# Kernel tuning notes

Measured on AMD Instinct MI355X. Metric: run time of the kernel, lower is better.

The kernel has to match this reference:

```python
import jax, jax.numpy as jnp
import numpy as np

EPS = 1e-5  # torch BatchNorm1d default eps
N0, N, ORIG, F, K, H, NC = 16, 96, 92, 64, 41, 128, 3


def _bn(x, g, b, axes):
    # training-mode batchnorm: biased batch stats over `axes`, per-channel affine
    m = jnp.mean(x, axis=axes, keepdims=True)
    v = jnp.mean((x - m) ** 2, axis=axes, keepdims=True)
    return (x - m) / jnp.sqrt(v + EPS) * g + b


def setup_inputs() -> dict:
    key = jax.random.key(0)
    ks = jax.random.split(key, 16)
    s = 0.05
    return {
        "atom_fea": jax.random.normal(ks[0], (N0, N, ORIG), jnp.float32),
        "nbr_fea": jax.random.normal(ks[1], (N0, N, N, K), jnp.float32),
        "adj": jax.random.randint(ks[2], (N0, N, N), 0, 2, jnp.int64),
        "emb_W": jax.random.normal(ks[3], (ORIG, F), jnp.float32) * s,
        "emb_b": jnp.zeros((F,), jnp.float32),
        "conv_W": jax.random.normal(ks[4], (NC, 2 * F + K, 2 * F), jnp.float32) * s,
        "conv_b": jnp.zeros((NC, 2 * F), jnp.float32),
        "bn1_g": jnp.ones((NC, 2 * F), jnp.float32),
        "bn1_b": jnp.zeros((NC, 2 * F), jnp.float32),
        "bn2_g": jnp.ones((NC, F), jnp.float32),
        "bn2_b": jnp.zeros((NC, F), jnp.float32),
        "fc_W": jax.random.normal(ks[5], (F, H), jnp.float32) * s,
        "fc_b": jnp.zeros((H,), jnp.float32),
        "out_W": jax.random.normal(ks[6], (H, 1), jnp.float32) * s,
        "out_b": jnp.zeros((1,), jnp.float32),
    }


def reference(atom_fea, nbr_fea, adj, emb_W, emb_b, conv_W, conv_b,
              bn1_g, bn1_b, bn2_g, bn2_b, fc_W, fc_b, out_W, out_b):
    fea = atom_fea @ emb_W + emb_b                       # (N0, N, F)
    adjf = adj.astype(fea.dtype)[..., None]              # (N0, N, N, 1)
    for i in range(NC):
        # NOTE: faithful to source - both FEA and masked term broadcast atom j's
        # own features along the neighbor axis (unsqueeze(2) in torch code).
        FEA = jnp.broadcast_to(fea[:, :, None, :], (N0, N, N, F))
        total = jnp.concatenate([FEA, adjf * FEA, nbr_fea], axis=3)   # (N0,N,N,2F+K)
        gated = total @ conv_W[i] + conv_b[i]                         # (N0,N,N,2F)
        gated = _bn(gated, bn1_g[i], bn1_b[i], (0, 1, 2))
        filt, core = jnp.split(gated, 2, axis=3)
        summed = jnp.sum(jax.nn.sigmoid(filt) * jax.nn.softplus(core), axis=2)  # (N0,N,F)
        summed = _bn(summed, bn2_g[i], bn2_b[i], (0, 1))
        fea = jax.nn.softplus(fea + summed)
    crys = jnp.mean(fea, axis=1)                                      # (N0, F)
    crys = jax.nn.softplus(jax.nn.softplus(crys) @ fc_W + fc_b)       # (N0, H)
    return crys @ out_W + out_b                                       # (N0, 1)
```

## Files before the change

kernel.cpp:

```cpp
#include <hip/hip_runtime.h>
#include <math.h>

#define N0c   16
#define NAt   96
#define ORIG  92
#define Fc    64
#define Kc    41
#define Hc    128
#define NCc   3
#define C2    128
#define EPSBN 1e-5f
#define JG    4
#define JPW   (NAt / JG)
#define NREP  32
#define SRL_STRIDE 12288
#define AROW  72
#define WFRAG 16384
#define INV1  (1.f / (float)(N0c * NAt * NAt))
#define INV2  (1.f / (float)(N0c * NAt))

typedef __attribute__((ext_vector_type(8))) short short8_t;
typedef __attribute__((ext_vector_type(4))) float f32x4;

__device__ __forceinline__ float sp_(float x){
    return fmaxf(x, 0.f) + __logf(1.f + __expf(-fabsf(x)));
}
__device__ __forceinline__ float sgm_(float x){
    return 1.f / (1.f + __expf(-x));
}
__device__ __forceinline__ unsigned short bfhi(float x){
    union { float f; unsigned u; } v; v.f = x;
    unsigned r = v.u + 0x7fff + ((v.u >> 16) & 1);
    return (unsigned short)(r >> 16);
}
__device__ __forceinline__ float bf2f(unsigned short h){
    union { float f; unsigned u; } v; v.u = ((unsigned)h) << 16; return v.f;
}

__global__ __launch_bounds__(256) void k_embed(const float* __restrict__ atom,
                                               const float* __restrict__ W,
                                               const float* __restrict__ b,
                                               float* __restrict__ fea){
    int row = blockIdx.x * 4 + (threadIdx.x >> 6);
    int f   = threadIdx.x & 63;
    const float* ar = atom + row * ORIG;
    float acc = b[f];
    #pragma unroll 4
    for (int o = 0; o < ORIG; ++o) acc += ar[o] * W[o * Fc + f];
    fea[row * Fc + f] = acc;
}

__global__ __launch_bounds__(256) void k_pre(const float* __restrict__ nbr,
                                             const int*   __restrict__ adj,
                                             float* __restrict__ ST,
                                             float* __restrict__ cntf){
    int r    = blockIdx.x;
    int lane = threadIdx.x & 63;
    int jg   = __builtin_amdgcn_readfirstlane(threadIdx.x >> 6);
    __shared__ float rS[JG][Kc], rT[JG][Kc], rc[JG];
    float S = 0.f, T = 0.f, cn = 0.f;
    int j0 = jg * JPW;
    for (int j = j0; j < j0 + JPW; ++j){
        float a = (float)adj[r * NAt + j];
        float v = (lane < Kc) ? nbr[((size_t)r * NAt + j) * Kc + lane] : 0.f;
        S += v; T += a * v; cn += a;
    }
    if (lane < Kc){ rS[jg][lane] = S; rT[jg][lane] = T; }
    if (lane == 0) rc[jg] = cn;
    __syncthreads();
    int t = threadIdx.x;
    if (t < Kc){
        ST[r * (2 * Kc) + t]      = rS[0][t] + rS[1][t] + rS[2][t] + rS[3][t];
        ST[r * (2 * Kc) + Kc + t] = rT[0][t] + rT[1][t] + rT[2][t] + rT[3][t];
    }
    if (t == 0) cntf[r] = rc[0] + rc[1] + rc[2] + rc[3];
}

__global__ __launch_bounds__(128) void k_gram(const float* __restrict__ nbr,
                                              float* __restrict__ pG, int rpb){
    int blk = blockIdx.x;
    int t   = threadIdx.x;
    int k   = (t % 21) * 2;
    int lb  = (t / 21) * 7;
    __shared__ float L[NAt * Kc];
    float a0[7] = {0,0,0,0,0,0,0}, a1[7] = {0,0,0,0,0,0,0};
    for (int rr = 0; rr < rpb; ++rr){
        int r = blk * rpb + rr;
        __syncthreads();
        for (int i = t; i < NAt * Kc; i += 128)
            L[i] = nbr[(size_t)r * NAt * Kc + i];
        __syncthreads();
        if (t < 126){
            for (int j = 0; j < NAt; ++j){
                float vk0 = L[j * Kc + k];
                float vk1 = (k + 1 < Kc) ? L[j * Kc + k + 1] : 0.f;
                #pragma unroll
                for (int m = 0; m < 7; ++m){
                    if (lb + m < Kc){
                        float lv = L[j * Kc + lb + m];
                        a0[m] += vk0 * lv;
                        a1[m] += vk1 * lv;
                    }
                }
            }
        }
    }
    if (t < 126){
        float* dst = pG + (size_t)blk * (Kc * Kc);
        #pragma unroll
        for (int m = 0; m < 7; ++m){
            if (lb + m < Kc){
                dst[k * Kc + lb + m] = a0[m];
                if (k + 1 < Kc) dst[(k + 1) * Kc + lb + m] = a1[m];
            }
        }
    }
}

__global__ __launch_bounds__(64) void k_gred(const float* __restrict__ pG,
                                             float* __restrict__ G){
    int i  = (blockIdx.x % 27) * 64 + threadIdx.x;
    int b0 = (blockIdx.x / 27) * 96;
    if (i < Kc * Kc){
        float s = 0.f;
        #pragma unroll 4
        for (int b = b0; b < b0 + 96; ++b) s += pG[(size_t)b * (Kc * Kc) + i];
        atomicAdd(&G[i], s);
    }
}

__global__ void k_wt(const float* __restrict__ convW, float* __restrict__ W3T){
    int l = blockIdx.x, c = threadIdx.x;
    const float* Wl = convW + (size_t)l * 169 * C2;
    float* dst = W3T + ((size_t)l * C2 + c) * 44;
    for (int k = 0; k < Kc; ++k) dst[k] = Wl[(C2 + k) * C2 + c];
    dst[41] = 0.f; dst[42] = 0.f; dst[43] = 0.f;
}

__global__ __launch_bounds__(256) void k_wtb(const float* __restrict__ convW,
                                             unsigned short* __restrict__ W3F){
    int l = blockIdx.x;
    const float* Wl = convW + (size_t)l * 169 * C2;
    for (int it = 0; it < 8; ++it){
        int idx  = threadIdx.x + it * 256;
        int lane = idx & 63;
        int fid  = idx >> 6;
        int h    = fid & 1;
        int ks   = (fid >> 1) & 1;
        int nt   = fid >> 2;
        int n    = nt * 16 + (lane & 15);
        unsigned short* dst = W3F + (size_t)l * WFRAG + fid * 512 + lane * 8;
        #pragma unroll
        for (int i = 0; i < 8; ++i){
            int k = ks * 32 + (lane >> 4) * 8 + i;
            float w = (k < Kc) ? Wl[(C2 + k) * C2 + n] : 0.f;
            unsigned short hi = bfhi(w);
            dst[i] = h ? bfhi(w - bf2f(hi)) : hi;
        }
    }
}

__global__ __launch_bounds__(128) void k_quad(const float* __restrict__ G,
                                              const float* __restrict__ convW,
                                              float* __restrict__ q3){
    int l = blockIdx.x, c = threadIdx.x;
    const float* Wl = convW + (size_t)l * 169 * C2;
    __shared__ float GL[Kc * Kc];
    for (int i = c; i < Kc * Kc; i += 128) GL[i] = G[i];
    float w3[Kc];
    #pragma unroll
    for (int k = 0; k < Kc; ++k) w3[k] = Wl[(C2 + k) * C2 + c];
    __syncthreads();
    float q = 0.f;
    for (int k = 0; k < Kc; ++k){
        float gw = 0.f;
        #pragma unroll
        for (int m = 0; m < Kc; ++m) gw += GL[k * Kc + m] * w3[m];
        q += w3[k] * gw;
    }
    q3[l * C2 + c] = q;
}

__global__ __launch_bounds__(128)
void k_front(float* __restrict__ fea,
             const float* __restrict__ Wl,
             const float* __restrict__ bl,
             const float* __restrict__ W3Tl,
             const float* __restrict__ ST,
             const float* __restrict__ cntf,
             float* __restrict__ p1,
             float* __restrict__ p2,
             float* __restrict__ sum1R,
             float* __restrict__ sq1R,
             const float* __restrict__ summed,
             const float* __restrict__ sum2Rp,
             const float* __restrict__ sq2Rp,
             const float* __restrict__ g2p,
             const float* __restrict__ b2p,
             int upd){
    int c  = threadIdx.x;
    int r0 = blockIdx.x * 2;
    __shared__ float F2[2][Fc];
    __shared__ float A2L[Fc], B2L[Fc];

    if (upd){
        if (c < Fc){
            float s = 0.f, q = 0.f;
            for (int rr = 0; rr < NREP; ++rr){
                s += sum2Rp[rr * Fc + c];
                q += sq2Rp[rr * Fc + c];
            }
            float m = s * INV2;
            float v = q * INV2 - m * m;
            float A = g2p[c] * rsqrtf(v + EPSBN);
            A2L[c] = A;
            B2L[c] = b2p[c] - m * A;
        }
        __syncthreads();
        {
            int rr = c >> 6, cc = c & 63;
            int r  = r0 + rr;
            float nv = sp_(fea[r * Fc + cc] + summed[r * Fc + cc] * A2L[cc] + B2L[cc]);
            F2[rr][cc] = nv;
            fea[r * Fc + cc] = nv;
        }
        __syncthreads();
    } else {
        int rr = c >> 6, cc = c & 63;
        F2[rr][cc] = fea[(r0 + rr) * Fc + cc];
        __syncthreads();
    }

    float w3[Kc];
    const float* wt = W3Tl + c * 44;
    #pragma unroll
    for (int k = 0; k < 40; k += 4){
        float4 v = *(const float4*)(wt + k);
        w3[k] = v.x; w3[k+1] = v.y; w3[k+2] = v.z; w3[k+3] = v.w;
    }
    w3[40] = wt[40];
    float s1 = 0.f, q1 = 0.f;
    for (int rr = 0; rr < 2; ++rr){
        int r = r0 + rr;
        float a1 = bl[c], a2 = 0.f;
        #pragma unroll 8
        for (int f = 0; f < Fc; ++f){
            float fv = F2[rr][f];
            a1 += fv * Wl[f * C2 + c];
            a2 += fv * Wl[(Fc + f) * C2 + c];
        }
        p1[r * C2 + c] = a1;
        p2[r * C2 + c] = a2;
        const float* Sr = ST + r * (2 * Kc);
        const float* Tr = Sr + Kc;
        float u = 0.f, tt = 0.f;
        #pragma unroll
        for (int k = 0; k < Kc; ++k){ u += Sr[k] * w3[k]; tt += Tr[k] * w3[k]; }
        float cn = cntf[r];
        s1 += (float)NAt * a1 + cn * a2 + u;
        q1 += (float)NAt * a1 * a1 + cn * a2 * a2
            + 2.f * cn * a1 * a2 + 2.f * a1 * u + 2.f * a2 * tt;
    }
    int slot = blockIdx.x & (NREP - 1);
    atomicAdd(&sum1R[slot * C2 + c], s1);
    atomicAdd(&sq1R[slot * C2 + c], q1);
}

__global__ __launch_bounds__(512)
void k_apply(const float* __restrict__ nbr,
             const int*   __restrict__ adj,
             const unsigned short* __restrict__ W3Fl,
             const float* __restrict__ p1,
             const float* __restrict__ p2,
             const float* __restrict__ sum1R,
             const float* __restrict__ sq1R,
             const float* __restrict__ qv,
             const float* __restrict__ g1,
             const float* __restrict__ b1,
             float* __restrict__ summed,
             float* __restrict__ sum2R,
             float* __restrict__ sq2R){
    int r    = blockIdx.x;
    int tid  = threadIdx.x;
    int lane = tid & 63;
    int w    = __builtin_amdgcn_readfirstlane(tid >> 6);
    int ntF  = w & 3;
    int mh   = w >> 2;

    __shared__ unsigned short sAH[NAt * AROW];
    __shared__ unsigned short sAL[NAt * AROW];
    __shared__ float AJ[NAt];
    __shared__ float PL1[C2], PL2[C2], A1L[C2], B1L[C2];
    __shared__ float TpW[8][16];

    short8_t BH[2][2], BL[2][2];
    #pragma unroll
    for (int ni = 0; ni < 2; ++ni){
        int nt = ntF + ni * 4;
        #pragma unroll
        for (int ks = 0; ks < 2; ++ks){
            int fidH = (nt * 2 + ks) * 2;
            BH[ni][ks] = *(const short8_t*)(W3Fl + fidH * 512 + lane * 8);
            BL[ni][ks] = *(const short8_t*)(W3Fl + (fidH + 1) * 512 + lane * 8);
        }
    }

    const float* nb = nbr + (size_t)r * (NAt * Kc);
    for (int idx = tid; idx < NAt * Kc; idx += 512){
        int j = idx / Kc, k = idx - j * Kc;
        float x = nb[idx];
        unsigned short hi = bfhi(x);
        sAH[j * AROW + k] = hi;
        sAL[j * AROW + k] = bfhi(x - bf2f(hi));
    }
    for (int idx = tid; idx < NAt * 23; idx += 512){
        int j = idx / 23, k = Kc + (idx - j * 23);
        sAH[j * AROW + k] = 0;
        sAL[j * AROW + k] = 0;
    }
    if (tid < C2){
        int c = tid;
        float s = 0.f, q = 0.f;
        for (int rr = 0; rr < NREP; ++rr){ s += sum1R[rr * C2 + c]; q += sq1R[rr * C2 + c]; }
        float m = s * INV1;
        float v = (q + qv[c]) * INV1 - m * m;
        float A = g1[c] * rsqrtf(v + EPSBN);
        A1L[c] = A;
        B1L[c] = b1[c] - m * A;
    } else if (tid < 256){
        PL1[tid - 128] = p1[r * C2 + tid - 128];
    } else if (tid < 384){
        PL2[tid - 256] = p2[r * C2 + tid - 256];
    } else if (tid < 480){
        AJ[tid - 384] = (float)adj[r * NAt + tid - 384];
    }
    __syncthreads();

    f32x4 acc[3][2] = {};
    int q4 = (lane >> 4) * 8;
    #pragma unroll
    for (int mt = 0; mt < 3; ++mt){
        int jrow = (mh * 48 + mt * 16 + (lane & 15)) * AROW;
        short8_t AH0 = *(const short8_t*)(&sAH[jrow + q4]);
        short8_t AH1 = *(const short8_t*)(&sAH[jrow + 32 + q4]);
        short8_t AL0 = *(const short8_t*)(&sAL[jrow + q4]);
        short8_t AL1 = *(const short8_t*)(&sAL[jrow + 32 + q4]);
        #pragma unroll
        for (int ni = 0; ni < 2; ++ni){
            acc[mt][ni] = __builtin_amdgcn_mfma_f32_16x16x32_bf16(AH0, BH[ni][0], acc[mt][ni], 0, 0, 0);
            acc[mt][ni] = __builtin_amdgcn_mfma_f32_16x16x32_bf16(AH0, BL[ni][0], acc[mt][ni], 0, 0, 0);
            acc[mt][ni] = __builtin_amdgcn_mfma_f32_16x16x32_bf16(AL0, BH[ni][0], acc[mt][ni], 0, 0, 0);
            acc[mt][ni] = __builtin_amdgcn_mfma_f32_16x16x32_bf16(AH1, BH[ni][1], acc[mt][ni], 0, 0, 0);
            acc[mt][ni] = __builtin_amdgcn_mfma_f32_16x16x32_bf16(AH1, BL[ni][1], acc[mt][ni], 0, 0, 0);
            acc[mt][ni] = __builtin_amdgcn_mfma_f32_16x16x32_bf16(AL1, BH[ni][1], acc[mt][ni], 0, 0, 0);
        }
    }

    int cF = ntF * 16 + (lane & 15);
    int cC = cF + 64;
    float p1F = PL1[cF], p2F = PL2[cF], A1F = A1L[cF], B1F = B1L[cF];
    float p1C = PL1[cC], p2C = PL2[cC], A1C = A1L[cC], B1C = B1L[cC];
    float tsum = 0.f;
    #pragma unroll
    for (int mt = 0; mt < 3; ++mt){
        #pragma unroll
        for (int rg = 0; rg < 4; ++rg){
            int j = mh * 48 + mt * 16 + (lane >> 4) * 4 + rg;
            float ajf = AJ[j];
            float gf = (p1F + ajf * p2F + acc[mt][0][rg]) * A1F + B1F;
            float gc = (p1C + ajf * p2C + acc[mt][1][rg]) * A1C + B1C;
            tsum += sgm_(gf) * sp_(gc);
        }
    }
    tsum += __shfl_xor(tsum, 16);
    tsum += __shfl_xor(tsum, 32);
    if (lane < 16) TpW[w][lane] = tsum;
    __syncthreads();
    if (tid < Fc){
        int f = tid;
        float s = TpW[f >> 4][f & 15] + TpW[(f >> 4) + 4][f & 15];
        summed[r * Fc + f] = s;
        int slot = blockIdx.x & (NREP - 1);
        atomicAdd(&sum2R[slot * Fc + f], s);
        atomicAdd(&sq2R[slot * Fc + f], s * s);
    }
}

__global__ __launch_bounds__(128) void k_final(const float* __restrict__ fea,
                                               const float* __restrict__ summed,
                                               const float* __restrict__ sum2R,
                                               const float* __restrict__ sq2R,
                                               const float* __restrict__ g2,
                                               const float* __restrict__ b2,
                                               const float* __restrict__ fcW,
                                               const float* __restrict__ fcb,
                                               const float* __restrict__ outW,
                                               const float* __restrict__ outb,
                                               float* __restrict__ out){
    int b = blockIdx.x;
    int t = threadIdx.x;
    __shared__ float spc[Fc];
    __shared__ float red[Hc];
    if (t < Fc){
        float s = 0.f, q = 0.f;
        for (int r = 0; r < NREP; ++r){ s += sum2R[r * Fc + t]; q += sq2R[r * Fc + t]; }
        float m  = s * INV2;
        float v  = q * INV2 - m * m;
        float A2 = g2[t] * rsqrtf(v + EPSBN);
        float B2 = b2[t] - m * A2;
        float acc = 0.f;
        for (int i = 0; i < NAt; ++i){
            int idx = (b * NAt + i) * Fc + t;
            acc += sp_(fea[idx] + summed[idx] * A2 + B2);
        }
        spc[t] = sp_(acc * (1.f / NAt));
    }
    __syncthreads();
    float h = fcb[t];
    #pragma unroll 4
    for (int f = 0; f < Fc; ++f) h += spc[f] * fcW[f * Hc + t];
    h = sp_(h);
    red[t] = h * outW[t];
    __syncthreads();
    for (int off = 64; off > 0; off >>= 1){
        if (t < off) red[t] += red[t + off];
        __syncthreads();
    }
    if (t == 0) out[b] = red[0] + outb[0];
}

extern "C" void kernel_launch(void* const* d_in, const int* in_sizes, int n_in,
                              void* d_out, int out_size, void* d_ws, size_t ws_size,
                              hipStream_t stream){
    const float* atom  = (const float*)d_in[0];
    const float* nbr   = (const float*)d_in[1];
    const int*   adj   = (const int*)  d_in[2];
    const float* embW  = (const float*)d_in[3];
    const float* embB  = (const float*)d_in[4];
    const float* convW = (const float*)d_in[5];
    const float* convB = (const float*)d_in[6];
    const float* bn1g  = (const float*)d_in[7];
    const float* bn1b  = (const float*)d_in[8];
    const float* bn2g  = (const float*)d_in[9];
    const float* bn2b  = (const float*)d_in[10];
    const float* fcW   = (const float*)d_in[11];
    const float* fcb   = (const float*)d_in[12];
    const float* outW  = (const float*)d_in[13];
    const float* outb  = (const float*)d_in[14];
    float* out = (float*)d_out;
    float* ws  = (float*)d_ws;

    const int ROWS = N0c * NAt;
    float* fea    = ws;
    float* p1     = ws + 98304;
    float* p2     = ws + 294912;
    float* summed = ws + 491520;
    float* SRL    = ws + 589824;
    float* ST     = ws + 626688;
    float* cntf   = ws + 752640;
    float* q3     = ws + 754176;
    float* W3T    = ws + 754560;
    unsigned short* W3F = (unsigned short*)(ws + 771456);
    const size_t PERS = 796032;

    size_t ws_f = ws_size / sizeof(float);
    int nblk; float *pG, *G;
    if (ws_f >= PERS + (size_t)1536 * 1681 + 1681 + 64){
        nblk = 1536; pG = ws + PERS; G = pG + (size_t)nblk * 1681;
    } else if (ws_f >= PERS + (size_t)768 * 1681 + 1681 + 64){
        nblk = 768;  pG = ws + PERS; G = pG + (size_t)nblk * 1681;
    } else if (ws_f >= PERS + (size_t)384 * 1681 + 1681 + 64){
        nblk = 384;  pG = ws + PERS; G = pG + (size_t)nblk * 1681;
    } else {
        nblk = 384;  pG = ws;        G = ws + 650000;
    }
    int rpb = 1536 / nblk;
    int ph  = nblk / 96;

    hipMemsetAsync(G, 0, Kc * Kc * sizeof(float), stream);
    k_gram <<<nblk, 128, 0, stream>>>(nbr, pG, rpb);
    k_gred <<<27 * ph, 64, 0, stream>>>(pG, G);
    k_wt   <<<NCc, C2, 0, stream>>>(convW, W3T);
    k_wtb  <<<NCc, 256, 0, stream>>>(convW, W3F);
    k_quad <<<NCc, C2, 0, stream>>>(G, convW, q3);
    k_embed<<<ROWS / 4, 256, 0, stream>>>(atom, embW, embB, fea);
    k_pre  <<<ROWS, 256, 0, stream>>>(nbr, adj, ST, cntf);
    hipMemsetAsync(SRL, 0, 3 * SRL_STRIDE * sizeof(float), stream);

    for (int l = 0; l < NCc; ++l){
        const float* Wl   = convW + (size_t)l * 169 * C2;
        const float* bl   = convB + l * C2;
        const float* W3Tl = W3T + (size_t)l * C2 * 44;
        const unsigned short* W3Fl = W3F + (size_t)l * WFRAG;
        float* sum1R = SRL + l * SRL_STRIDE;
        float* sq1R  = sum1R + 4096;
        float* sum2R = sum1R + 8192;
        float* sq2R  = sum1R + 10240;
        const float* sum2Rp = (l > 0) ? SRL + (l - 1) * SRL_STRIDE + 8192 : SRL;
        const float* sq2Rp  = (l > 0) ? SRL + (l - 1) * SRL_STRIDE + 10240 : SRL;
        const float* g2p    = bn2g + (l > 0 ? (l - 1) : 0) * Fc;
        const float* b2p    = bn2b + (l > 0 ? (l - 1) : 0) * Fc;

        k_front <<<ROWS / 2, C2, 0, stream>>>(fea, Wl, bl, W3Tl, ST, cntf,
                                              p1, p2, sum1R, sq1R,
                                              summed, sum2Rp, sq2Rp, g2p, b2p,
                                              l > 0 ? 1 : 0);
        k_apply <<<ROWS, 512, 0, stream>>>(nbr, adj, W3Fl, p1, p2,
                                           sum1R, sq1R, q3 + l * C2,
                                           bn1g + l * C2, bn1b + l * C2,
                                           summed, sum2R, sq2R);
    }

    k_final<<<N0c, Hc, 0, stream>>>(fea, summed,
                                    SRL + 2 * SRL_STRIDE + 8192,
                                    SRL + 2 * SRL_STRIDE + 10240,
                                    bn2g + 2 * Fc, bn2b + 2 * Fc,
                                    fcW, fcb, outW, outb, out);
}
```

Baseline: 292.6 us.

## Replace scalar per-row front kernel with split-bf16 MFMA block GEMM

Replaces the scalar k_front kernel, which runs two rows per 128-thread block, with k_pgemm. The new kernel processes 16 rows per 512-thread block and computes p1, p2 and the nbr projections u and tt as one GEMM on bf16 MFMA instructions. Three-term hi/lo bf16 splitting keeps the result close to fp32 accuracy. A new prep kernel packs the weights into MFMA fragment layout, and BN1 partial stats are reduced with shuffles before the atomics. This is meant to cut the front-stage compute cost, at the price of extra prep work and some precision loss from the bf16 split.

```diff
diff --git a/kernel.cpp b/kernel.cpp
--- a/kernel.cpp
+++ b/kernel.cpp
@@ -16,6 +16,9 @@
 #define SRL_STRIDE 12288
 #define AROW  72
 #define WFRAG 16384
+#define PROW  200
+#define DROW  516
+#define PGFRAG (32 * 2 * 2 * 512)
 #define INV1  (1.f / (float)(N0c * NAt * NAt))
 #define INV2  (1.f / (float)(N0c * NAt))
 
@@ -129,14 +132,6 @@
     }
 }
 
-__global__ void k_wt(const float* __restrict__ convW, float* __restrict__ W3T){
-    int l = blockIdx.x, c = threadIdx.x;
-    const float* Wl = convW + (size_t)l * 169 * C2;
-    float* dst = W3T + ((size_t)l * C2 + c) * 44;
-    for (int k = 0; k < Kc; ++k) dst[k] = Wl[(C2 + k) * C2 + c];
-    dst[41] = 0.f; dst[42] = 0.f; dst[43] = 0.f;
-}
-
 __global__ __launch_bounds__(256) void k_wtb(const float* __restrict__ convW,
                                              unsigned short* __restrict__ W3F){
     int l = blockIdx.x;
@@ -160,6 +155,32 @@
     }
 }
 
+__global__ __launch_bounds__(64) void k_wtb2(const float* __restrict__ convW,
+                                             unsigned short* __restrict__ W3F2){
+    int l  = blockIdx.x >> 5;
+    int nt = blockIdx.x & 31;
+    const float* Wl = convW + (size_t)l * 169 * C2;
+    int lane = threadIdx.x;
+    int kb = (nt < 16) ? 0 : (nt < 24 ? 64 : 128);
+    for (int f = 0; f < 4; ++f){
+        int ks2 = f >> 1, h = f & 1;
+        unsigned short* dst = W3F2 + (size_t)l * PGFRAG
+                            + (((size_t)nt * 2 + ks2) * 2 + h) * 512 + lane * 8;
+        #pragma unroll
+        for (int i = 0; i < 8; ++i){
+            int kabs = kb + ks2 * 32 + (lane >> 4) * 8 + i;
+            int n    = nt * 16 + (lane & 15);
+            float wv = 0.f;
+            if (nt < 8)        wv = Wl[kabs * C2 + n];
+            else if (nt < 16)  wv = Wl[(64 + kabs) * C2 + (n - 128)];
+            else if (nt < 24){ int kk = kabs - 64;  if (kk < Kc) wv = Wl[(C2 + kk) * C2 + (n - 256)]; }
+            else             { int kk = kabs - 128; if (kk < Kc) wv = Wl[(C2 + kk) * C2 + (n - 384)]; }
+            unsigned short hi = bfhi(wv);
+            dst[i] = h ? bfhi(wv - bf2f(hi)) : hi;
+        }
+    }
+}
+
 __global__ __launch_bounds__(128) void k_quad(const float* __restrict__ G,
                                               const float* __restrict__ convW,
                                               float* __restrict__ q3){
@@ -181,89 +202,129 @@
     q3[l * C2 + c] = q;
 }
 
-__global__ __launch_bounds__(128)
-void k_front(float* __restrict__ fea,
-             const float* __restrict__ Wl,
+__global__ __launch_bounds__(512)
+void k_pgemm(float* __restrict__ fea,
              const float* __restrict__ bl,
-             const float* __restrict__ W3Tl,
+             const unsigned short* __restrict__ Bf,
              const float* __restrict__ ST,
              const float* __restrict__ cntf,
-             float* __restrict__ p1,
-             float* __restrict__ p2,
-             float* __restrict__ sum1R,
-             float* __restrict__ sq1R,
              const float* __restrict__ summed,
              const float* __restrict__ sum2Rp,
              const float* __restrict__ sq2Rp,
              const float* __restrict__ g2p,
              const float* __restrict__ b2p,
+             float* __restrict__ p1,
+             float* __restrict__ p2,
+             float* __restrict__ sum1R,
+             float* __restrict__ sq1R,
              int upd){
-    int c  = threadIdx.x;
-    int r0 = blockIdx.x * 2;
-    __shared__ float F2[2][Fc];
-    __shared__ float A2L[Fc], B2L[Fc];
-
-    if (upd){
-        if (c < Fc){
-            float s = 0.f, q = 0.f;
-            for (int rr = 0; rr < NREP; ++rr){
-                s += sum2Rp[rr * Fc + c];
-                q += sq2Rp[rr * Fc + c];
+    int r0   = blockIdx.x * 16;
+    int tid  = threadIdx.x;
+    int lane = tid & 63;
+    int w    = __builtin_amdgcn_readfirstlane(tid >> 6);
+    __shared__ unsigned short AH[16 * PROW], AL[16 * PROW];
+    __shared__ float Db[16 * DROW];
+    __shared__ float A2L[Fc], B2L[Fc], cnL[16];
+
+    if (upd && tid < Fc){
+        float s = 0.f, q = 0.f;
+        for (int rr = 0; rr < NREP; ++rr){
+            s += sum2Rp[rr * Fc + tid];
+            q += sq2Rp[rr * Fc + tid];
+        }
+        float m = s * INV2;
+        float v = q * INV2 - m * m;
+        float A = g2p[tid] * rsqrtf(v + EPSBN);
+        A2L[tid] = A;
+        B2L[tid] = b2p[tid] - m * A;
+    }
+    if (tid < 16) cnL[tid] = cntf[r0 + tid];
+    __syncthreads();
+
+    for (int idx = tid; idx < 16 * 192; idx += 512){
+        int r = idx / 192, k = idx - r * 192;
+        int gr = r0 + r;
+        float v = 0.f;
+        if (k < 64){
+            v = fea[gr * Fc + k];
+            if (upd){
+                v = sp_(v + summed[gr * Fc + k] * A2L[k] + B2L[k]);
+                fea[gr * Fc + k] = v;
             }
-            float m = s * INV2;
-            float v = q * INV2 - m * m;
-            float A = g2p[c] * rsqrtf(v + EPSBN);
-            A2L[c] = A;
-            B2L[c] = b2p[c] - m * A;
-        }
-        __syncthreads();
-        {
-            int rr = c >> 6, cc = c & 63;
-            int r  = r0 + rr;
-            float nv = sp_(fea[r * Fc + cc] + summed[r * Fc + cc] * A2L[cc] + B2L[cc]);
-            F2[rr][cc] = nv;
-            fea[r * Fc + cc] = nv;
-        }
-        __syncthreads();
-    } else {
-        int rr = c >> 6, cc = c & 63;
-        F2[rr][cc] = fea[(r0 + rr) * Fc + cc];
-        __syncthreads();
-    }
-
-    float w3[Kc];
-    const float* wt = W3Tl + c * 44;
+        } else if (k < 105){
+            v = ST[gr * (2 * Kc) + (k - 64)];
+        } else if (k >= 128 && k < 169){
+            v = ST[gr * (2 * Kc) + Kc + (k - 128)];
+        }
+        unsigned short hi = bfhi(v);
+        AH[r * PROW + k] = hi;
+        AL[r * PROW + k] = bfhi(v - bf2f(hi));
+    }
+    __syncthreads();
+
+    int q8   = (lane >> 4) * 8;
+    int mrow = lane & 15;
+    int kb   = (w < 4) ? 0 : (w < 6 ? 64 : 128);
+    short8_t AH0 = *(const short8_t*)(&AH[mrow * PROW + kb + q8]);
+    short8_t AH1 = *(const short8_t*)(&AH[mrow * PROW + kb + 32 + q8]);
+    short8_t AL0 = *(const short8_t*)(&AL[mrow * PROW + kb + q8]);
+    short8_t AL1 = *(const short8_t*)(&AL[mrow * PROW + kb + 32 + q8]);
+    f32x4 acc[4] = {};
     #pragma unroll
-    for (int k = 0; k < 40; k += 4){
-        float4 v = *(const float4*)(wt + k);
-        w3[k] = v.x; w3[k+1] = v.y; w3[k+2] = v.z; w3[k+3] = v.w;
-    }
-    w3[40] = wt[40];
-    float s1 = 0.f, q1 = 0.f;
-    for (int rr = 0; rr < 2; ++rr){
-        int r = r0 + rr;
-        float a1 = bl[c], a2 = 0.f;
-        #pragma unroll 8
-        for (int f = 0; f < Fc; ++f){
-            float fv = F2[rr][f];
-            a1 += fv * Wl[f * C2 + c];
-            a2 += fv * Wl[(Fc + f) * C2 + c];
-        }
-        p1[r * C2 + c] = a1;
-        p2[r * C2 + c] = a2;
-        const float* Sr = ST + r * (2 * Kc);
-        const float* Tr = Sr + Kc;
-        float u = 0.f, tt = 0.f;
-        #pragma unroll
-        for (int k = 0; k < Kc; ++k){ u += Sr[k] * w3[k]; tt += Tr[k] * w3[k]; }
-        float cn = cntf[r];
-        s1 += (float)NAt * a1 + cn * a2 + u;
-        q1 += (float)NAt * a1 * a1 + cn * a2 * a2
-            + 2.f * cn * a1 * a2 + 2.f * a1 * u + 2.f * a2 * tt;
-    }
-    int slot = blockIdx.x & (NREP - 1);
-    atomicAdd(&sum1R[slot * C2 + c], s1);
-    atomicAdd(&sq1R[slot * C2 + c], q1);
+    for (int nti = 0; nti < 4; ++nti){
+        int nt = w * 4 + nti;
+        const unsigned short* base = Bf + ((size_t)nt * 2) * 2 * 512;
+        short8_t BH0 = *(const short8_t*)(base + 0 * 512 + lane * 8);
+        short8_t BL0 = *(const short8_t*)(base + 1 * 512 + lane * 8);
+        short8_t BH1 = *(const short8_t*)(base + 2 * 512 + lane * 8);
+        short8_t BL1 = *(const short8_t*)(base + 3 * 512 + lane * 8);
+        acc[nti] = __builtin_amdgcn_mfma_f32_16x16x32_bf16(AH0, BH0, acc[nti], 0, 0, 0);
+        acc[nti] = __builtin_amdgcn_mfma_f32_16x16x32_bf16(AH0, BL0, acc[nti], 0, 0, 0);
+        acc[nti] = __builtin_amdgcn_mfma_f32_16x16x32_bf16(AL0, BH0, acc[nti], 0, 0, 0);
+        acc[nti] = __builtin_amdgcn_mfma_f32_16x16x32_bf16(AH1, BH1, acc[nti], 0, 0, 0);
+        acc[nti] = __builtin_amdgcn_mfma_f32_16x16x32_bf16(AH1, BL1, acc[nti], 0, 0, 0);
+        acc[nti] = __builtin_amdgcn_mfma_f32_16x16x32_bf16(AL1, BH1, acc[nti], 0, 0, 0);
+    }
+    #pragma unroll
+    for (int nti = 0; nti < 4; ++nti){
+        int col = (w * 4 + nti) * 16 + mrow;
+        #pragma unroll
+        for (int rg = 0; rg < 4; ++rg){
+            int row = (lane >> 4) * 4 + rg;
+            Db[row * DROW + col] = acc[nti][rg];
+        }
+    }
+    __syncthreads();
+
+    {
+        int c = tid >> 2, rq = tid & 3;
+        float blc = bl[c];
+        float s1 = 0.f, q1 = 0.f;
+        #pragma unroll
+        for (int i = 0; i < 4; ++i){
+            int r = rq * 4 + i;
+            float a1 = Db[r * DROW + c] + blc;
+            float a2 = Db[r * DROW + 128 + c];
+            float u  = Db[r * DROW + 256 + c];
+            float tt = Db[r * DROW + 384 + c];
+            float cn = cnL[r];
+            s1 += (float)NAt * a1 + cn * a2 + u;
+            q1 += (float)NAt * a1 * a1 + cn * a2 * a2
+                + 2.f * cn * a1 * a2 + 2.f * a1 * u + 2.f * a2 * tt;
+        }
+        s1 += __shfl_xor(s1, 1);  s1 += __shfl_xor(s1, 2);
+        q1 += __shfl_xor(q1, 1);  q1 += __shfl_xor(q1, 2);
+        if (rq == 0){
+            int slot = blockIdx.x & (NREP - 1);
+            atomicAdd(&sum1R[slot * C2 + c], s1);
+            atomicAdd(&sq1R[slot * C2 + c], q1);
+        }
+    }
+    for (int idx = tid; idx < 16 * 256; idx += 512){
+        int r = idx >> 8, cc = idx & 255;
+        if (cc < 128) p1[(r0 + r) * C2 + cc]        = Db[r * DROW + cc] + bl[cc];
+        else          p2[(r0 + r) * C2 + (cc - 128)] = Db[r * DROW + cc];
+    }
 }
 
 __global__ __launch_bounds__(512)
@@ -459,9 +520,9 @@
     float* ST     = ws + 626688;
     float* cntf   = ws + 752640;
     float* q3     = ws + 754176;
-    float* W3T    = ws + 754560;
-    unsigned short* W3F = (unsigned short*)(ws + 771456);
-    const size_t PERS = 796032;
+    unsigned short* W3F  = (unsigned short*)(ws + 754560);
+    unsigned short* W3F2 = (unsigned short*)(ws + 779136);
+    const size_t PERS = 877440;
 
     size_t ws_f = ws_size / sizeof(float);
     int nblk; float *pG, *G;
@@ -480,18 +541,17 @@
     hipMemsetAsync(G, 0, Kc * Kc * sizeof(float), stream);
     k_gram <<<nblk, 128, 0, stream>>>(nbr, pG, rpb);
     k_gred <<<27 * ph, 64, 0, stream>>>(pG, G);
-    k_wt   <<<NCc, C2, 0, stream>>>(convW, W3T);
     k_wtb  <<<NCc, 256, 0, stream>>>(convW, W3F);
+    k_wtb2 <<<NCc * 32, 64, 0, stream>>>(convW, W3F2);
     k_quad <<<NCc, C2, 0, stream>>>(G, convW, q3);
     k_embed<<<ROWS / 4, 256, 0, stream>>>(atom, embW, embB, fea);
     k_pre  <<<ROWS, 256, 0, stream>>>(nbr, adj, ST, cntf);
     hipMemsetAsync(SRL, 0, 3 * SRL_STRIDE * sizeof(float), stream);
 
     for (int l = 0; l < NCc; ++l){
-        const float* Wl   = convW + (size_t)l * 169 * C2;
-        const float* bl   = convB + l * C2;
-        const float* W3Tl = W3T + (size_t)l * C2 * 44;
-        const unsigned short* W3Fl = W3F + (size_t)l * WFRAG;
+        const float* bl    = convB + l * C2;
+        const unsigned short* W3Fl  = W3F  + (size_t)l * WFRAG;
+        const unsigned short* W3F2l = W3F2 + (size_t)l * PGFRAG;
         float* sum1R = SRL + l * SRL_STRIDE;
         float* sq1R  = sum1R + 4096;
         float* sum2R = sum1R + 8192;
@@ -501,10 +561,10 @@
         const float* g2p    = bn2g + (l > 0 ? (l - 1) : 0) * Fc;
         const float* b2p    = bn2b + (l > 0 ? (l - 1) : 0) * Fc;
 
-        k_front <<<ROWS / 2, C2, 0, stream>>>(fea, Wl, bl, W3Tl, ST, cntf,
-                                              p1, p2, sum1R, sq1R,
-                                              summed, sum2Rp, sq2Rp, g2p, b2p,
-                                              l > 0 ? 1 : 0);
+        k_pgemm <<<ROWS / 16, 512, 0, stream>>>(fea, bl, W3F2l, ST, cntf,
+                                                summed, sum2Rp, sq2Rp, g2p, b2p,
+                                                p1, p2, sum1R, sq1R,
+                                                l > 0 ? 1 : 0);
         k_apply <<<ROWS, 512, 0, stream>>>(nbr, adj, W3Fl, p1, p2,
                                            sum1R, sq1R, q3 + l * C2,
                                            bn1g + l * C2, bn1b + l * C2,
```

Result: slower. 304.1 us (+3.9%).
